# Kernel tuning notes

Hardware: AMD Instinct MI355X
Metric: run time of the kernel (lower is better)

## Reference

```python
import jax, jax.numpy as jnp
import numpy as np

N, D, H, B, HID, E = 4096, 64, 4, 4, 64, 32768
NEG_SLOPE = 0.2


def setup_inputs() -> dict:
    key = jax.random.key(0)
    ks = jax.random.split(key, 24)
    s = 0.05
    emb = jax.random.normal(ks[0], (N, D), jnp.float32)
    src = jax.random.randint(ks[1], (E,), 0, N)
    dst = jax.random.randint(ks[2], (E,), 0, N)
    bond = jax.random.randint(ks[3], (E,), 0, B)
    # append self-loops (bond type 0) so every softmax row has a finite entry
    loop = jnp.arange(N)
    src = jnp.concatenate([src, loop])
    dst = jnp.concatenate([dst, loop])
    bond = jnp.concatenate([bond, jnp.zeros((N,), bond.dtype)])
    return {
        'embeddings': emb,
        'Qw': jax.random.normal(ks[4], (D, D), jnp.float32) * s,
        'Qb': jnp.zeros((D,), jnp.float32),
        'Kw': jax.random.normal(ks[5], (D, D), jnp.float32) * s,
        'Kb': jnp.zeros((D,), jnp.float32),
        'Vw': jax.random.normal(ks[6], (D, D), jnp.float32) * s,
        'Vb': jnp.zeros((D,), jnp.float32),
        'W0': jax.random.normal(ks[7], (B, H, 2 * D, HID), jnp.float32) * s,
        'b0': jnp.zeros((B, H, HID), jnp.float32),
        'W1': jax.random.normal(ks[8], (B, H, HID, HID), jnp.float32) * s,
        'b1': jnp.zeros((B, H, HID), jnp.float32),
        'W2': jax.random.normal(ks[9], (B, H, HID), jnp.float32) * s,
        'b2': jnp.zeros((B, H), jnp.float32),
        'Pw': jax.random.normal(ks[10], (H * D, D), jnp.float32) * s,
        'Pb': jnp.zeros((D,), jnp.float32),
        'src': src,
        'dst': dst,
        'bond': bond,
    }


def reference(embeddings, Qw, Qb, Kw, Kb, Vw, Vb, W0, b0, W1, b1, W2, b2, Pw, Pb, src, dst, bond):
    n, d = embeddings.shape
    nb, nh = W0.shape[0], W0.shape[1]
    Q = embeddings @ Qw + Qb
    K = embeddings @ Kw + Kb
    V = embeddings @ Vw + Vb
    # symmetric scatter: scores for both (src->dst) and (dst->src)
    s_all = jnp.concatenate([src, dst])
    d_all = jnp.concatenate([dst, src])
    b_all = jnp.concatenate([bond, bond])
    x = jnp.concatenate([Q[s_all], K[d_all]], axis=-1)  # [2E', 2D]

    def mlp_scores(bt):
        h = jax.nn.relu(jnp.einsum('ef,hfk->ehk', x, W0[bt]) + b0[bt])
        h = jax.nn.relu(jnp.einsum('ehk,hkj->ehj', h, W1[bt]) + b1[bt])
        sc = jnp.einsum('ehk,hk->eh', h, W2[bt]) + b2[bt]
        return jax.nn.leaky_relu(sc, NEG_SLOPE)

    scores = jnp.zeros((x.shape[0], nh), x.dtype)
    for bt in range(nb):  # small fixed loop over bond types (grouped GEMMs)
        scores = jnp.where((b_all == bt)[:, None], mlp_scores(bt), scores)

    S = jnp.full((nh, n, n), -jnp.inf, embeddings.dtype)
    S = S.at[:, s_all, d_all].set(scores.T)  # [H, N, N]
    A = jax.nn.softmax(S, axis=-1)
    out = jnp.einsum('hij,jd->hid', A, V)  # [H, N, D]
    out = out.transpose(1, 0, 2).reshape(n, nh * d)
    return out @ Pw + Pb
```

## Files before the change

### kernel.cpp

```cpp
#include <hip/hip_runtime.h>
#include <hip/hip_bf16.h>
#include <math.h>

#define D 64
#define H 4
#define NB 4
#define TILE 64
#define PAD 128
#define NEG_SLOPE 0.2f

typedef __attribute__((ext_vector_type(8))) short short8;
typedef __attribute__((ext_vector_type(4))) float f32x4;

__device__ __forceinline__ unsigned short f2bf(float f) {
    union { float f; unsigned int u; } c; c.f = f;
    const unsigned int u = c.u;
    return (unsigned short)((u + 0x7fffu + ((u >> 16) & 1u)) >> 16);
}

__global__ __launch_bounds__(256) void prep_kernel(
    const float* __restrict__ emb,
    const float* __restrict__ Qw, const float* __restrict__ Qb,
    const float* __restrict__ Kw, const float* __restrict__ Kb,
    const float* __restrict__ Vw, const float* __restrict__ Vb,
    unsigned short* __restrict__ Qbf, unsigned short* __restrict__ Kbf,
    float* __restrict__ V,
    const float* __restrict__ W0, const float* __restrict__ W1,
    unsigned short* __restrict__ W0p, unsigned short* __restrict__ W1p,
    const int* __restrict__ bond, int Ep, int TE,
    int* __restrict__ rowFill, int* __restrict__ blockBondCnt, int nblk,
    int N, int nq)
{
    const int tid = threadIdx.x;
    const int bid = blockIdx.x;
    if (bid < nq) {
        const int gz = bid * 256 + tid;
        if (gz < N) rowFill[gz] = 0;
        __shared__ float e[4][64];
        const int n = bid * 4 + (tid >> 6);
        const int d = tid & 63;
        if (n < N) e[tid >> 6][d] = emb[n * D + d];
        __syncthreads();
        if (n < N) {
            float aq = Qb[d], ak = Kb[d], av = Vb[d];
            const float* er = e[tid >> 6];
#pragma unroll 8
            for (int k = 0; k < D; ++k) {
                const float x = er[k];
                aq += x * Qw[k * D + d];
                ak += x * Kw[k * D + d];
                av += x * Vw[k * D + d];
            }
            Qbf[n * D + d] = f2bf(aq);
            Kbf[n * D + d] = f2bf(ak);
            V[n * D + d] = av;
        }
    } else if (bid < nq + 512) {
        const int idx = (bid - nq) * 256 + tid;
        {
            const int j = idx & 7, ln = (idx >> 3) & 63, nt = (idx >> 9) & 3;
            const int ks = (idx >> 11) & 3, bh = idx >> 13;
            const int k = ks * 32 + ((ln >> 4) << 3) + j;
            const int nn = (nt << 4) + (ln & 15);
            W0p[idx] = f2bf(W0[((size_t)bh * 128 + k) * 64 + nn]);
        }
        if (idx < 65536) {
            const int j = idx & 7, ln = (idx >> 3) & 63, nt = (idx >> 9) & 3;
            const int ks = (idx >> 11) & 1, bh = idx >> 12;
            const int k = ks * 32 + ((ln >> 4) << 3) + j;
            const int nn = (nt << 4) + (ln & 15);
            W1p[idx] = f2bf(W1[((size_t)bh * 64 + k) * 64 + nn]);
        }
    } else {
        __shared__ int wcnt[4][NB];
        const int vb = bid - nq - 512;
        const int e = vb * 256 + tid;
        const int lane = tid & 63, wave = tid >> 6;
        int bt = -1;
        if (e < TE) bt = (e < Ep) ? bond[e] : bond[e - Ep];
#pragma unroll
        for (int t = 0; t < NB; ++t) {
            const unsigned long long m = __ballot(bt == t);
            if (lane == 0) wcnt[wave][t] = (int)__popcll(m);
        }
        __syncthreads();
        if (tid < NB) {
            int s = 0;
#pragma unroll
            for (int w = 0; w < 4; ++w) s += wcnt[w][tid];
            blockBondCnt[tid * nblk + vb] = s;
        }
    }
}

__global__ __launch_bounds__(256) void scatter_kernel(
    const int* __restrict__ src, const int* __restrict__ dst,
    const int* __restrict__ bond, int Ep, int TE, int nblk,
    const int* __restrict__ blockBondCnt, int* __restrict__ rowFill,
    int* __restrict__ edge_col, int* __restrict__ edge_eid,
    int* __restrict__ padPos, int* __restrict__ bond_edges, int* __restrict__ bondOff)
{
    __shared__ int chunkpre[256];
    __shared__ int base_lds[NB];
    __shared__ int wcnt[4][NB], wbase[4][NB];
    const int tid = threadIdx.x;
    const int vb = blockIdx.x;
    const int M = NB * nblk;
    const int c = (M + 255) >> 8;

    int s = 0;
    for (int i = 0; i < c; ++i) { const int idx = tid * c + i; if (idx < M) s += blockBondCnt[idx]; }
    chunkpre[tid] = s;
    __syncthreads();
    int val = s;
    for (int off = 1; off < 256; off <<= 1) {
        const int o = (tid >= off) ? chunkpre[tid - off] : 0;
        __syncthreads();
        val += o;
        chunkpre[tid] = val;
        __syncthreads();
    }
    int excl = val - s;
    for (int i = 0; i < c; ++i) {
        const int idx = tid * c + i;
        if (idx < M) {
            const int t = idx / nblk, r = idx - t * nblk;
            if (r == vb) base_lds[t] = excl;
            if (vb == 0 && r == 0) bondOff[t] = excl;
            excl += blockBondCnt[idx];
        }
    }
    if (vb == 0 && tid == 255) bondOff[NB] = chunkpre[255];
    __syncthreads();

    const int lane = tid & 63, wave = tid >> 6;
    const int e = vb * 256 + tid;
    const bool act = (e < TE);
    int sN = 0, dN = 0, bt = -1;
    if (act) {
        if (e < Ep) { sN = src[e]; dN = dst[e]; bt = bond[e]; }
        else        { sN = dst[e - Ep]; dN = src[e - Ep]; bt = bond[e - Ep]; }
        const int p = atomicAdd(&rowFill[sN], 1);
        if (p < PAD) {
            edge_col[sN * PAD + p] = dN;
            edge_eid[sN * PAD + p] = e;
            padPos[e] = sN * PAD + p;
        } else padPos[e] = -1;
    }
    int myrank = 0;
#pragma unroll
    for (int t = 0; t < NB; ++t) {
        const unsigned long long m = __ballot(bt == t);
        if (lane == 0) wcnt[wave][t] = (int)__popcll(m);
        if (bt == t) myrank = (int)__popcll(m & ((1ull << lane) - 1ull));
    }
    __syncthreads();
    if (tid < NB) {
        int sum = 0;
#pragma unroll
        for (int w = 0; w < 4; ++w) { wbase[w][tid] = sum; sum += wcnt[w][tid]; }
    }
    __syncthreads();
    if (act) bond_edges[base_lds[bt] + wbase[wave][bt] + myrank] = e;
}

__global__ __launch_bounds__(256) void mlp_kernel(
    const unsigned short* __restrict__ Qbf, const unsigned short* __restrict__ Kbf,
    const int* __restrict__ src, const int* __restrict__ dst, int Ep,
    const int* __restrict__ bondOff, const int* __restrict__ bond_edges,
    const int* __restrict__ padPos,
    const unsigned short* __restrict__ W0p, const unsigned short* __restrict__ W1p,
    const float* __restrict__ b0, const float* __restrict__ b1,
    const float* __restrict__ W2, const float* __restrict__ b2,
    float* __restrict__ S)
{
    const int bt = blockIdx.y;
    const int base = bondOff[bt];
    const int cnt  = bondOff[bt + 1] - base;
    const int t0 = blockIdx.x * TILE;
    if (t0 >= cnt) return;
    const int ne = min(TILE, cnt - t0);

    __shared__ __align__(16) unsigned char xs[64 * 256];
    __shared__ __align__(16) unsigned char h0s[4][64 * 128];
    __shared__ int eids[TILE];

    const int tid = threadIdx.x;
    if (tid < TILE) eids[tid] = (tid < ne) ? bond_edges[base + t0 + tid] : 0;
    __syncthreads();

    for (int i = tid; i < 1024; i += 256) {
        const int el = i >> 4, u = i & 15;
        uint4 v = make_uint4(0, 0, 0, 0);
        if (el < ne) {
            const int e = eids[el];
            int s, d;
            if (e < Ep) { s = src[e]; d = dst[e]; }
            else        { s = dst[e - Ep]; d = src[e - Ep]; }
            v = (u < 8) ? ((const uint4*)(Qbf + s * 64))[u]
                        : ((const uint4*)(Kbf + d * 64))[u - 8];
        }
        const int b = (el << 8) + (u << 4);
        *(uint4*)(xs + (b ^ ((el & 7) << 4))) = v;
    }
    __syncthreads();

    const int lane = tid & 63;
    const int h = tid >> 6;
    const int bh = bt * H + h;
    const int lg = lane >> 4;
    const int lr = lane & 15;

    f32x4 acc[4][4];
    const float* bb0 = b0 + bh * 64;
#pragma unroll
    for (int nt = 0; nt < 4; ++nt) {
        const float bv = bb0[(nt << 4) + lr];
#pragma unroll
        for (int mt = 0; mt < 4; ++mt) acc[mt][nt] = (f32x4){bv, bv, bv, bv};
    }
    const short8* W0f = (const short8*)W0p + (size_t)bh * 1024;
#pragma unroll
    for (int ks = 0; ks < 4; ++ks) {
        short8 a[4];
        const int koff = (ks << 6) + (lg << 4);
#pragma unroll
        for (int mt = 0; mt < 4; ++mt) {
            const int row = (mt << 4) + lr;
            const int b = (row << 8) + koff;
            a[mt] = *(const short8*)(xs + (b ^ ((row & 7) << 4)));
        }
        short8 bfr[4];
#pragma unroll
        for (int nt = 0; nt < 4; ++nt) bfr[nt] = W0f[(((ks << 2) + nt) << 6) + lane];
#pragma unroll
        for (int mt = 0; mt < 4; ++mt)
#pragma unroll
            for (int nt = 0; nt < 4; ++nt)
                acc[mt][nt] = __builtin_amdgcn_mfma_f32_16x16x32_bf16(a[mt], bfr[nt], acc[mt][nt], 0, 0, 0);
    }
    unsigned char* h0 = h0s[h];
#pragma unroll
    for (int mt = 0; mt < 4; ++mt)
#pragma unroll
        for (int nt = 0; nt < 4; ++nt)
#pragma unroll
            for (int r = 0; r < 4; ++r) {
                const int row = (mt << 4) + (lg << 2) + r;
                const int col = (nt << 4) + lr;
                const int b = (row << 7) + (col << 1);
                *(unsigned short*)(h0 + (b ^ ((row & 7) << 4))) = f2bf(fmaxf(acc[mt][nt][r], 0.f));
            }

    f32x4 acc1[4][4];
    const float* bb1 = b1 + bh * 64;
#pragma unroll
    for (int nt = 0; nt < 4; ++nt) {
        const float bv = bb1[(nt << 4) + lr];
#pragma unroll
        for (int mt = 0; mt < 4; ++mt) acc1[mt][nt] = (f32x4){bv, bv, bv, bv};
    }
    const short8* W1f = (const short8*)W1p + (size_t)bh * 512;
#pragma unroll
    for (int ks = 0; ks < 2; ++ks) {
        short8 a[4];
        const int koff = (ks << 6) + (lg << 4);
#pragma unroll
        for (int mt = 0; mt < 4; ++mt) {
            const int row = (mt << 4) + lr;
            const int b = (row << 7) + koff;
            a[mt] = *(const short8*)(h0 + (b ^ ((row & 7) << 4)));
        }
        short8 bfr[4];
#pragma unroll
        for (int nt = 0; nt < 4; ++nt) bfr[nt] = W1f[(((ks << 2) + nt) << 6) + lane];
#pragma unroll
        for (int mt = 0; mt < 4; ++mt)
#pragma unroll
            for (int nt = 0; nt < 4; ++nt)
                acc1[mt][nt] = __builtin_amdgcn_mfma_f32_16x16x32_bf16(a[mt], bfr[nt], acc1[mt][nt], 0, 0, 0);
    }

    const float* w2 = W2 + bh * 64;
    float w2v[4];
#pragma unroll
    for (int nt = 0; nt < 4; ++nt) w2v[nt] = w2[(nt << 4) + lr];
    float p[4][4];
#pragma unroll
    for (int mt = 0; mt < 4; ++mt)
#pragma unroll
        for (int r = 0; r < 4; ++r) {
            float s = 0.f;
#pragma unroll
            for (int nt = 0; nt < 4; ++nt) s += fmaxf(acc1[mt][nt][r], 0.f) * w2v[nt];
            p[mt][r] = s;
        }
#pragma unroll
    for (int off = 1; off <= 8; off <<= 1)
#pragma unroll
        for (int mt = 0; mt < 4; ++mt)
#pragma unroll
            for (int r = 0; r < 4; ++r) p[mt][r] += __shfl_xor(p[mt][r], off, 64);
    const int e_w = ((lr >> 2) << 4) + (lg << 2) + (lr & 3);
    float sc = p[lr >> 2][lr & 3] + b2[bh];
    sc = sc > 0.f ? sc : NEG_SLOPE * sc;
    if (e_w < ne) {
        const int pp = padPos[eids[e_w]];
        if (pp >= 0) S[(size_t)pp * H + h] = sc;
    }
}

__global__ __launch_bounds__(256) void agg_kernel(
    const float* __restrict__ V, const float* __restrict__ S,
    const int* __restrict__ rowFill,
    const int* __restrict__ edge_col, const int* __restrict__ edge_eid,
    const float* __restrict__ Pw, const float* __restrict__ Pb, float* __restrict__ out)
{
    const int row = blockIdx.x;
    const int tid = threadIdx.x;
    const int lane = tid & 63;
    const int h = tid >> 6;
    const int beg = row * PAD;
    int deg = rowFill[row];
    if (deg > PAD) deg = PAD;

    __shared__ int tcol[PAD], teid[PAD], scol[PAD], spos[PAD], win[PAD];
    __shared__ float wgt[4][PAD];
    __shared__ float rr[256];
    __shared__ float part2[4][64];

    for (int a = tid; a < deg; a += 256) { tcol[a] = edge_col[beg + a]; teid[a] = edge_eid[beg + a]; }
    __syncthreads();
    for (int a = tid; a < deg; a += 256) {
        const int e = teid[a];
        int r = 0;
        for (int b = 0; b < deg; ++b) r += (teid[b] < e);
        scol[r] = tcol[a];
        spos[r] = a;
    }
    __syncthreads();
    for (int a = tid; a < deg; a += 256) {
        const int c = scol[a];
        int wn = 1;
        for (int b = a + 1; b < deg; ++b) if (scol[b] == c) { wn = 0; break; }
        win[a] = wn;
    }
    __syncthreads();

    float m = -1e30f;
    for (int a = lane; a < deg; a += 64)
        if (win[a]) m = fmaxf(m, S[(size_t)(beg + spos[a]) * H + h]);
#pragma unroll
    for (int off = 32; off; off >>= 1) m = fmaxf(m, __shfl_xor(m, off, 64));

    float dn = 0.f;
    for (int a = lane; a < deg; a += 64) {
        const float wv = win[a] ? __expf(S[(size_t)(beg + spos[a]) * H + h] - m) : 0.f;
        wgt[h][a] = wv;
        dn += wv;
    }
#pragma unroll
    for (int off = 32; off; off >>= 1) dn += __shfl_xor(dn, off, 64);

    float accv = 0.f;
    for (int a = 0; a < deg; ++a) accv += wgt[h][a] * V[(size_t)scol[a] * D + lane];
    rr[tid] = accv / dn;
    __syncthreads();
    {
        float sps = 0.f;
#pragma unroll 8
        for (int k = 0; k < 64; ++k) sps += rr[h * 64 + k] * Pw[(h * 64 + k) * D + lane];
        part2[h][lane] = sps;
    }
    __syncthreads();
    if (tid < 64)
        out[(size_t)row * D + tid] = part2[0][tid] + part2[1][tid] + part2[2][tid] + part2[3][tid] + Pb[tid];
}

extern "C" void kernel_launch(void* const* d_in, const int* in_sizes, int n_in,
                              void* d_out, int out_size, void* d_ws, size_t ws_size,
                              hipStream_t stream)
{
    const float* emb = (const float*)d_in[0];
    const float* Qw  = (const float*)d_in[1];
    const float* Qb  = (const float*)d_in[2];
    const float* Kw  = (const float*)d_in[3];
    const float* Kb  = (const float*)d_in[4];
    const float* Vw  = (const float*)d_in[5];
    const float* Vb  = (const float*)d_in[6];
    const float* W0  = (const float*)d_in[7];
    const float* b0  = (const float*)d_in[8];
    const float* W1  = (const float*)d_in[9];
    const float* b1  = (const float*)d_in[10];
    const float* W2  = (const float*)d_in[11];
    const float* b2  = (const float*)d_in[12];
    const float* Pw  = (const float*)d_in[13];
    const float* Pb  = (const float*)d_in[14];
    const int* src   = (const int*)d_in[15];
    const int* dst   = (const int*)d_in[16];
    const int* bond  = (const int*)d_in[17];

    const int N  = in_sizes[0] / D;
    const int Ep = in_sizes[15];
    const int TE = 2 * Ep;
    const int nblk = (TE + 255) / 256;
    const int nq = (N + 3) / 4;

    char* w = (char*)d_ws;
    auto alloc = [&](size_t bytes) -> void* {
        void* p = (void*)w;
        w += ((bytes + 255) / 256) * 256;
        return p;
    };
    unsigned short* Qbf = (unsigned short*)alloc((size_t)N * D * 2);
    unsigned short* Kbf = (unsigned short*)alloc((size_t)N * D * 2);
    float* V        = (float*)alloc((size_t)N * D * 4);
    unsigned short* W0p = (unsigned short*)alloc((size_t)131072 * 2);
    unsigned short* W1p = (unsigned short*)alloc((size_t)65536 * 2);
    float* S        = (float*)alloc((size_t)N * PAD * H * 4);
    int* edge_col   = (int*)alloc((size_t)N * PAD * 4);
    int* edge_eid   = (int*)alloc((size_t)N * PAD * 4);
    int* bond_edges = (int*)alloc((size_t)TE * 4);
    int* padPos     = (int*)alloc((size_t)TE * 4);
    int* blockBondCnt = (int*)alloc((size_t)NB * nblk * 4);
    int* bondOff    = (int*)alloc((size_t)(NB + 1) * 4);
    int* rowFill    = (int*)alloc((size_t)N * 4);
    if ((size_t)(w - (char*)d_ws) > ws_size) return;

    prep_kernel<<<nq + 512 + nblk, 256, 0, stream>>>(
        emb, Qw, Qb, Kw, Kb, Vw, Vb, Qbf, Kbf, V, W0, W1, W0p, W1p,
        bond, Ep, TE, rowFill, blockBondCnt, nblk, N, nq);
    scatter_kernel<<<nblk, 256, 0, stream>>>(
        src, dst, bond, Ep, TE, nblk, blockBondCnt, rowFill,
        edge_col, edge_eid, padPos, bond_edges, bondOff);
    dim3 mgrid((TE + TILE - 1) / TILE, NB);
    mlp_kernel<<<mgrid, 256, 0, stream>>>(
        Qbf, Kbf, src, dst, Ep, bondOff, bond_edges, padPos,
        W0p, W1p, b0, b1, W2, b2, S);
    agg_kernel<<<N, 256, 0, stream>>>(
        V, S, rowFill, edge_col, edge_eid, Pw, Pb, (float*)d_out);
}
```

Before: 78.20 us.

## Alias MLP LDS buffers and split aggregation V-gather across waves by edge

The MLP kernel now reuses one 32KB shared buffer for both the gathered edge features and the per-head hidden activations, adding a barrier between the two uses. This halves shared memory per block (48KB to 32KB) so more blocks can be resident. The aggregation kernel changes from each wave looping over all edges for its own head to each wave handling every fourth edge for all four heads. Each V row is then loaded once instead of four times, at the cost of an extra shared-memory reduction and two more barriers.

```diff
diff --git a/kernel.cpp b/kernel.cpp
--- a/kernel.cpp
+++ b/kernel.cpp
@@ -181,8 +181,7 @@
     if (t0 >= cnt) return;
     const int ne = min(TILE, cnt - t0);
 
-    __shared__ __align__(16) unsigned char xs[64 * 256];
-    __shared__ __align__(16) unsigned char h0s[4][64 * 128];
+    __shared__ __align__(16) unsigned char buf[32768];
     __shared__ int eids[TILE];
 
     const int tid = threadIdx.x;
@@ -201,7 +200,7 @@
                         : ((const uint4*)(Kbf + d * 64))[u - 8];
         }
         const int b = (el << 8) + (u << 4);
-        *(uint4*)(xs + (b ^ ((el & 7) << 4))) = v;
+        *(uint4*)(buf + (b ^ ((el & 7) << 4))) = v;
     }
     __syncthreads();
 
@@ -228,7 +227,7 @@
         for (int mt = 0; mt < 4; ++mt) {
             const int row = (mt << 4) + lr;
             const int b = (row << 8) + koff;
-            a[mt] = *(const short8*)(xs + (b ^ ((row & 7) << 4)));
+            a[mt] = *(const short8*)(buf + (b ^ ((row & 7) << 4)));
         }
         short8 bfr[4];
 #pragma unroll
@@ -239,7 +238,8 @@
             for (int nt = 0; nt < 4; ++nt)
                 acc[mt][nt] = __builtin_amdgcn_mfma_f32_16x16x32_bf16(a[mt], bfr[nt], acc[mt][nt], 0, 0, 0);
     }
-    unsigned char* h0 = h0s[h];
+    __syncthreads();
+    unsigned char* h0 = buf + h * 8192;
 #pragma unroll
     for (int mt = 0; mt < 4; ++mt)
 #pragma unroll
@@ -319,13 +319,15 @@
     const int row = blockIdx.x;
     const int tid = threadIdx.x;
     const int lane = tid & 63;
-    const int h = tid >> 6;
+    const int wv = tid >> 6;
     const int beg = row * PAD;
     int deg = rowFill[row];
     if (deg > PAD) deg = PAD;
 
     __shared__ int tcol[PAD], teid[PAD], scol[PAD], spos[PAD], win[PAD];
     __shared__ float wgt[4][PAD];
+    __shared__ float sdn[4];
+    __shared__ float partv[4][4][64];
     __shared__ float rr[256];
     __shared__ float part2[4][64];
 
@@ -349,28 +351,44 @@
 
     float m = -1e30f;
     for (int a = lane; a < deg; a += 64)
-        if (win[a]) m = fmaxf(m, S[(size_t)(beg + spos[a]) * H + h]);
+        if (win[a]) m = fmaxf(m, S[(size_t)(beg + spos[a]) * H + wv]);
 #pragma unroll
     for (int off = 32; off; off >>= 1) m = fmaxf(m, __shfl_xor(m, off, 64));
 
     float dn = 0.f;
     for (int a = lane; a < deg; a += 64) {
-        const float wv = win[a] ? __expf(S[(size_t)(beg + spos[a]) * H + h] - m) : 0.f;
-        wgt[h][a] = wv;
-        dn += wv;
+        const float wvv = win[a] ? __expf(S[(size_t)(beg + spos[a]) * H + wv] - m) : 0.f;
+        wgt[wv][a] = wvv;
+        dn += wvv;
     }
 #pragma unroll
     for (int off = 32; off; off >>= 1) dn += __shfl_xor(dn, off, 64);
-
-    float accv = 0.f;
-    for (int a = 0; a < deg; ++a) accv += wgt[h][a] * V[(size_t)scol[a] * D + lane];
-    rr[tid] = accv / dn;
-    __syncthreads();
+    if (lane == 0) sdn[wv] = dn;
+    __syncthreads();
+
+    float pv0 = 0.f, pv1 = 0.f, pv2 = 0.f, pv3 = 0.f;
+    for (int a = wv; a < deg; a += 4) {
+        const float vr = V[(size_t)scol[a] * D + lane];
+        pv0 += wgt[0][a] * vr;
+        pv1 += wgt[1][a] * vr;
+        pv2 += wgt[2][a] * vr;
+        pv3 += wgt[3][a] * vr;
+    }
+    partv[wv][0][lane] = pv0;
+    partv[wv][1][lane] = pv1;
+    partv[wv][2][lane] = pv2;
+    partv[wv][3][lane] = pv3;
+    __syncthreads();
+
+    rr[wv * 64 + lane] = (partv[0][wv][lane] + partv[1][wv][lane]
+                        + partv[2][wv][lane] + partv[3][wv][lane]) / sdn[wv];
+    __syncthreads();
+
     {
         float sps = 0.f;
 #pragma unroll 8
-        for (int k = 0; k < 64; ++k) sps += rr[h * 64 + k] * Pw[(h * 64 + k) * D + lane];
-        part2[h][lane] = sps;
+        for (int k = 0; k < 64; ++k) sps += rr[wv * 64 + k] * Pw[(wv * 64 + k) * D + lane];
+        part2[wv][lane] = sps;
     }
     __syncthreads();
     if (tid < 64)
```

Result: no change. 77.91 us (-0.4%).
